# Kernel tuning notes

Measured on AMD Instinct MI355X. Metric: run time of the kernel, lower is better.

The kernel has to match this reference:

```python
import jax, jax.numpy as jnp
import numpy as np

B, S, D, H, DK, NQ, DFF = 4, 2048, 512, 8, 64, 4, 2048
EPS = 1e-5  # torch LayerNorm default


def setup_inputs() -> dict:
    key = jax.random.key(0)
    ks = jax.random.split(key, 8)
    sc = 1.0 / np.sqrt(D)
    inp = {"x": jax.random.normal(ks[0], (B, S, D), jnp.float32)}
    inp["wq"] = jax.random.normal(ks[1], (D, D), jnp.float32) * sc
    inp["bq"] = jnp.zeros((D,), jnp.float32)
    inp["wk"] = jax.random.normal(ks[2], (D, D), jnp.float32) * sc
    inp["bk"] = jnp.zeros((D,), jnp.float32)
    inp["wv"] = jax.random.normal(ks[3], (D, D), jnp.float32) * sc
    inp["bv"] = jnp.zeros((D,), jnp.float32)
    inp["wo"] = jax.random.normal(ks[4], (D, D), jnp.float32) * sc
    inp["bo"] = jnp.zeros((D,), jnp.float32)
    inp["w1"] = jax.random.normal(ks[5], (D, DFF), jnp.float32) * sc
    inp["b1"] = jnp.zeros((DFF,), jnp.float32)
    inp["w2"] = jax.random.normal(ks[6], (DFF, D), jnp.float32) * (1.0 / np.sqrt(DFF))
    inp["b2"] = jnp.zeros((D,), jnp.float32)
    inp["g1"] = jnp.ones((D,), jnp.float32)
    inp["be1"] = jnp.zeros((D,), jnp.float32)
    inp["g2"] = jnp.ones((D,), jnp.float32)
    inp["be2"] = jnp.zeros((D,), jnp.float32)
    return inp


def _layernorm(x, g, b):
    m = x.mean(-1, keepdims=True)
    v = ((x - m) ** 2).mean(-1, keepdims=True)
    return (x - m) * jax.lax.rsqrt(v + EPS) * g + b


def _forward(x, wq, bq, wk, bk, wv, bv, wo, bo, w1, b1, w2, b2, g1, be1, g2, be2):
    Bx, Sx, Dx = x.shape

    def heads(w, b):  # [B,S,D] -> [B,H,S,DK]
        return (x @ w + b).reshape(Bx, Sx, H, DK).transpose(0, 2, 1, 3)

    q, k, v = heads(wq, bq), heads(wk, bk), heads(wv, bv)
    # Quantum circuit 'execute' yields a uniform distribution over 2^NQ bitstrings,
    # so score = E_s[(qn.s)(kn.s)] = 0.25*(sum(qn)*sum(kn) + qn.kn) over the first
    # NQ components of each head slice (closed form of the original Python loops).
    qn, kn = q[..., :NQ], k[..., :NQ]
    scores = 0.25 * (
        qn.sum(-1)[..., :, None] * kn.sum(-1)[..., None, :]
        + jnp.einsum('bhin,bhjn->bhij', qn, kn)
    )
    attn = jax.nn.softmax(scores, axis=-1)  # [B,H,S,S]
    o = jnp.einsum('bhij,bhjd->bhid', attn, v)
    o = o.transpose(0, 2, 1, 3).reshape(Bx, Sx, Dx) @ wo + bo
    x1 = _layernorm(x + o, g1, be1)  # dropout is identity in eval
    ff = jax.nn.relu(x1 @ w1 + b1) @ w2 + b2
    return _layernorm(x1 + ff, g2, be2)


def reference(x, wq, bq, wk, bk, wv, bv, wo, bo, w1, b1, w2, b2, g1, be1, g2, be2):
    return _forward(x, wq, bq, wk, bk, wv, bv, wo, bo, w1, b1, w2, b2, g1, be1, g2, be2)
```

## Files before the change

kernel.cpp:

```cpp
#include <hip/hip_runtime.h>
#include <cstdint>

#define B_   4
#define S_   2048
#define D_   512
#define H_   8
#define DFF_ 2048

typedef __attribute__((ext_vector_type(4))) float  f32x4;
typedef __attribute__((ext_vector_type(4))) int    i32x4;
typedef __attribute__((ext_vector_type(2))) unsigned int u32x2;
typedef __attribute__((ext_vector_type(4))) unsigned int u32x4;
typedef __attribute__((ext_vector_type(8))) unsigned short u16x8;

__device__ inline void mfma_bf16(f32x4& acc, i32x4 a, i32x4 b) {
  asm("v_mfma_f32_16x16x32_bf16 %0, %1, %2, %0" : "+v"(acc) : "v"(a), "v"(b));
}
__device__ inline unsigned cvt_pk_bf16(float lo, float hi) {
  unsigned r;
  asm("v_cvt_pk_bf16_f32 %0, %1, %2" : "=v"(r) : "v"(lo), "v"(hi));
  return r;
}
__device__ inline unsigned short f2b(float f) {
  unsigned u = __builtin_bit_cast(unsigned, f);
  u += 0x7fffu + ((u >> 16) & 1u);
  return (unsigned short)(u >> 16);
}
__device__ inline float b2f(unsigned short u) {
  return __builtin_bit_cast(float, ((unsigned)u) << 16);
}
__device__ inline void gload_lds16(const void* g, void* l) {
  __builtin_amdgcn_global_load_lds(
      (const __attribute__((address_space(1))) void*)g,
      (__attribute__((address_space(3))) void*)l, 16, 0, 0);
}

__global__ __launch_bounds__(256) void convx_kernel(const float* __restrict__ x,
                                                    unsigned short* __restrict__ xb) {
  size_t i = ((size_t)blockIdx.x * 256 + threadIdx.x) * 8;
  f32x4 a = *(const f32x4*)(x + i);
  f32x4 b = *(const f32x4*)(x + i + 4);
  u32x4 o = {cvt_pk_bf16(a[0], a[1]), cvt_pk_bf16(a[2], a[3]),
             cvt_pk_bf16(b[0], b[1]), cvt_pk_bf16(b[2], b[3])};
  *(u32x4*)(xb + i) = o;
}

__global__ __launch_bounds__(256) void tconv_kernel(const float* __restrict__ src,
                                                    unsigned short* __restrict__ dst,
                                                    int RK, int CN) {
  __shared__ float t[64][65];
  const int tr0 = blockIdx.y * 64, tc0 = blockIdx.x * 64;
  const int c4 = (threadIdx.x & 15) * 4, rr = threadIdx.x >> 4;
#pragma unroll
  for (int i = 0; i < 4; ++i) {
    int r = i * 16 + rr;
    f32x4 v = *(const f32x4*)(src + (size_t)(tr0 + r) * CN + tc0 + c4);
    t[r][c4] = v[0]; t[r][c4 + 1] = v[1]; t[r][c4 + 2] = v[2]; t[r][c4 + 3] = v[3];
  }
  __syncthreads();
#pragma unroll
  for (int i = 0; i < 4; ++i) {
    int oc = i * 16 + rr;
    unsigned lo = cvt_pk_bf16(t[c4][oc], t[c4 + 1][oc]);
    unsigned hi = cvt_pk_bf16(t[c4 + 2][oc], t[c4 + 3][oc]);
    u32x2 pk = {lo, hi};
    *(u32x2*)(dst + (size_t)(tc0 + oc) * RK + tr0 + c4) = pk;
  }
}

__global__ __launch_bounds__(256) void wqk_kernel(const float* __restrict__ wq,
                                                  const float* __restrict__ bq,
                                                  const float* __restrict__ wk,
                                                  const float* __restrict__ bk,
                                                  unsigned short* __restrict__ wqkb,
                                                  float* __restrict__ biasqk) {
  int c = blockIdx.x;
  const float* w; const float* bb; int scol;
  if (c < 32) { w = wq; bb = bq; scol = (c >> 2) * 64 + (c & 3); }
  else { int c2 = c - 32; w = wk; bb = bk; scol = (c2 >> 2) * 64 + (c2 & 3); }
  for (int k = threadIdx.x; k < 512; k += 256)
    wqkb[c * 512 + k] = f2b(w[(size_t)k * 512 + scol]);
  if (threadIdx.x == 0) biasqk[c] = bb[scol];
}

template<int WM, int WN, int FM, int FN, int EPI>
__global__ __launch_bounds__(256) void gemm_kernel(
    const unsigned short* __restrict__ A, const unsigned short* __restrict__ Bt,
    const float* __restrict__ bias, void* __restrict__ Cout,
    int M, int N, int K) {
  constexpr int BM = WM * FM * 16, BN = WN * FN * 16;
  constexpr int ACH = BM * 4, TCH = (BM + BN) * 4;
  constexpr int BUFSZ = (BM + BN) * 64;
  __shared__ alignas(16) char lds[2][BUFSZ];
  const int tid = threadIdx.x, lane = tid & 63;
  const int wv = tid >> 6, wr = wv / WN, wc = wv % WN;
  const int bm0 = blockIdx.y * BM, bn0 = blockIdx.x * BN;
  const int l16 = lane & 15, lg = lane >> 4;

  auto stage = [&](int buf, int k0) {
#pragma unroll
    for (int i = 0; i < TCH / 256; ++i) {
      int ci = i * 256 + tid;
      const unsigned short* src;
      if (ci < ACH) {
        int r = ci >> 2, gs = ci & 3, g = gs ^ ((r >> 1) & 3);
        src = A + (size_t)(bm0 + r) * K + k0 + g * 8;
      } else {
        int cj = ci - ACH;
        int r = cj >> 2, gs = cj & 3, g = gs ^ ((r >> 1) & 3);
        src = Bt + (size_t)(bn0 + r) * K + k0 + g * 8;
      }
      gload_lds16(src, &lds[buf][ci * 16]);
    }
  };

  f32x4 acc[FM][FN];
#pragma unroll
  for (int i = 0; i < FM; ++i)
#pragma unroll
    for (int j = 0; j < FN; ++j) acc[i][j] = (f32x4){0.f, 0.f, 0.f, 0.f};

  stage(0, 0);
  __syncthreads();
  int cur = 0;
  for (int k0 = 0; k0 < K; k0 += 32) {
    if (k0 + 32 < K) stage(cur ^ 1, k0 + 32);

    i32x4 af[FM], bf[FN];
#pragma unroll
    for (int fm = 0; fm < FM; ++fm) {
      int r = wr * FM * 16 + fm * 16 + l16;
      int gs = lg ^ ((r >> 1) & 3);
      af[fm] = *(const i32x4*)(&lds[cur][r * 64 + gs * 16]);
    }
#pragma unroll
    for (int fn = 0; fn < FN; ++fn) {
      int r = wc * FN * 16 + fn * 16 + l16;
      int gs = lg ^ ((r >> 1) & 3);
      bf[fn] = *(const i32x4*)(&lds[cur][BM * 64 + r * 64 + gs * 16]);
    }
    __builtin_amdgcn_s_setprio(1);
#pragma unroll
    for (int fm = 0; fm < FM; ++fm)
#pragma unroll
      for (int fn = 0; fn < FN; ++fn)
        mfma_bf16(acc[fm][fn], af[fm], bf[fn]);
    __builtin_amdgcn_s_setprio(0);
    __syncthreads();
    cur ^= 1;
  }

#pragma unroll
  for (int fm = 0; fm < FM; ++fm) {
#pragma unroll
    for (int fn = 0; fn < FN; ++fn) {
      f32x4 a = acc[fm][fn];
      int gm = bm0 + wr * FM * 16 + fm * 16 + lg * 4;
      int gn = bn0 + wc * FN * 16 + fn * 16 + l16;
      float bz = bias[gn];
      if constexpr (EPI == 0) {
        float* C = (float*)Cout;
#pragma unroll
        for (int r = 0; r < 4; ++r) C[(size_t)(gm + r) * N + gn] = a[r] + bz;
      } else if constexpr (EPI == 1 || EPI == 2) {
        unsigned short* C = (unsigned short*)Cout;
#pragma unroll
        for (int r = 0; r < 4; ++r) {
          float v = a[r] + bz;
          if constexpr (EPI == 2) v = fmaxf(v, 0.f);
          C[(size_t)(gm + r) * N + gn] = f2b(v);
        }
      } else {
        unsigned short* C = (unsigned short*)Cout;
        int b = gm >> 11, s = gm & 2047;
        int h = gn >> 6, d = gn & 63;
        u32x2 pk = {cvt_pk_bf16(a[0] + bz, a[1] + bz),
                    cvt_pk_bf16(a[2] + bz, a[3] + bz)};
        *(u32x2*)(C + (((size_t)(b * 8 + h)) * 64 + d) * 2048 + s) = pk;
      }
    }
  }
}

__global__ __launch_bounds__(256) void qkfin_kernel(const float* __restrict__ qk,
                                                    float* __restrict__ qt,
                                                    float* __restrict__ kh) {
  int row = blockIdx.x * 4 + (threadIdx.x >> 6);
  int lane = threadIdx.x & 63;
  float v = qk[(size_t)row * 64 + lane];
  float s4 = v + __shfl_xor(v, 1);
  s4 += __shfl_xor(s4, 2);
  int b = row >> 11, s = row & 2047;
  if (lane < 32) {
    int h = lane >> 2, n = lane & 3;
    qt[(((size_t)(b * 8 + h)) * 2048 + s) * 4 + n] = 0.25f * v;
  } else {
    int c = lane - 32, h = c >> 2, n = c & 3;
    kh[(((size_t)(b * 8 + h)) * 2048 + s) * 4 + n] = v + s4;
  }
}

__global__ __launch_bounds__(256) void attn_kernel(
    const float* __restrict__ qt, const float* __restrict__ kh,
    const unsigned short* __restrict__ vt, unsigned short* __restrict__ O) {
  __shared__ alignas(16) char vlds[2][8192];
  const int tid = threadIdx.x, lane = tid & 63, wv = tid >> 6;
  const int L = blockIdx.x;
  const int x8 = L & 7, r8 = L >> 3;
  const int bh = x8 + 8 * (r8 & 3), qblk = r8 >> 2;
  const int b = bh >> 3, h = bh & 7;
  const int i0 = qblk * 64;
  const int l16 = lane & 15, g = lane >> 4;
  const int qrow = i0 + wv * 16 + l16;
  const float4 q = *(const float4*)(qt + ((size_t)bh * 2048 + qrow) * 4);
  const float* khb = kh + (size_t)bh * 2048 * 4;
  const unsigned short* vtb = vt + (size_t)bh * 64 * 2048;

  auto stage = [&](int buf, int j0) {
#pragma unroll
    for (int i = 0; i < 2; ++i) {
      int ci = i * 256 + tid;
      int d = ci >> 3, gs = ci & 7, gg = gs ^ (d & 7);
      gload_lds16(vtb + (size_t)d * 2048 + j0 + gg * 8, &vlds[buf][ci * 16]);
    }
  };

  f32x4 acc[4];
#pragma unroll
  for (int i = 0; i < 4; ++i) acc[i] = (f32x4){0.f, 0.f, 0.f, 0.f};
  float lsum = 0.f;

  stage(0, 0);
  __syncthreads();
  int cur = 0;
  for (int j0 = 0; j0 < S_; j0 += 64) {
    if (j0 + 64 < S_) stage(cur ^ 1, j0 + 64);

#pragma unroll
    for (int ks = 0; ks < 2; ++ks) {
      const int kbase = j0 + ks * 32 + g * 8;
      float p[8];
#pragma unroll
      for (int jj = 0; jj < 8; ++jj) {
        float4 kv = *(const float4*)(khb + (size_t)(kbase + jj) * 4);
        float s = q.x * kv.x + q.y * kv.y + q.z * kv.z + q.w * kv.w;
        p[jj] = __expf(s);
        lsum += p[jj];
      }
      i32x4 pb = {(int)cvt_pk_bf16(p[0], p[1]), (int)cvt_pk_bf16(p[2], p[3]),
                  (int)cvt_pk_bf16(p[4], p[5]), (int)cvt_pk_bf16(p[6], p[7])};
      __builtin_amdgcn_s_setprio(1);
#pragma unroll
      for (int dt = 0; dt < 4; ++dt) {
        int d = dt * 16 + l16;
        int gg = (ks * 4 + g) ^ (d & 7);
        i32x4 av = *(const i32x4*)(&vlds[cur][d * 128 + gg * 16]);
        mfma_bf16(acc[dt], av, pb);
      }
      __builtin_amdgcn_s_setprio(0);
    }
    __syncthreads();
    cur ^= 1;
  }

  lsum += __shfl_xor(lsum, 16);
  lsum += __shfl_xor(lsum, 32);
  const float rin = __fdividef(1.f, lsum);
  unsigned short* ob = O + ((size_t)(b * 2048 + qrow)) * 512 + h * 64;
#pragma unroll
  for (int dt = 0; dt < 4; ++dt) {
    f32x4 o = acc[dt] * rin;
    u32x2 pk = {cvt_pk_bf16(o[0], o[1]), cvt_pk_bf16(o[2], o[3])};
    *(u32x2*)(ob + dt * 16 + g * 4) = pk;
  }
}

__global__ __launch_bounds__(256) void ln1_kernel(const float* __restrict__ x,
                                                  const unsigned short* __restrict__ ob,
                                                  const float* __restrict__ g,
                                                  const float* __restrict__ be,
                                                  unsigned short* __restrict__ x1b) {
  const int row = blockIdx.x * 4 + (threadIdx.x >> 6), lane = threadIdx.x & 63;
  const float* xr = x + (size_t)row * 512 + lane * 8;
  f32x4 a0 = *(const f32x4*)xr, a1 = *(const f32x4*)(xr + 4);
  u16x8 rb = *(const u16x8*)(ob + (size_t)row * 512 + lane * 8);
  float v[8];
#pragma unroll
  for (int i = 0; i < 4; ++i) v[i] = a0[i] + b2f(rb[i]);
#pragma unroll
  for (int i = 0; i < 4; ++i) v[4 + i] = a1[i] + b2f(rb[4 + i]);
  float sum = 0.f;
#pragma unroll
  for (int i = 0; i < 8; ++i) sum += v[i];
#pragma unroll
  for (int m = 1; m < 64; m <<= 1) sum += __shfl_xor(sum, m);
  const float mean = sum * (1.f / 512.f);
  float vs = 0.f;
#pragma unroll
  for (int i = 0; i < 8; ++i) { v[i] -= mean; vs += v[i] * v[i]; }
#pragma unroll
  for (int m = 1; m < 64; m <<= 1) vs += __shfl_xor(vs, m);
  const float rs = rsqrtf(vs * (1.f / 512.f) + 1e-5f);
  const f32x4 g0 = *(const f32x4*)(g + lane * 8), g1 = *(const f32x4*)(g + lane * 8 + 4);
  const f32x4 b0 = *(const f32x4*)(be + lane * 8), b1 = *(const f32x4*)(be + lane * 8 + 4);
  float o[8];
#pragma unroll
  for (int i = 0; i < 4; ++i) o[i] = v[i] * rs * g0[i] + b0[i];
#pragma unroll
  for (int i = 0; i < 4; ++i) o[4 + i] = v[4 + i] * rs * g1[i] + b1[i];
  u32x4 pk = {cvt_pk_bf16(o[0], o[1]), cvt_pk_bf16(o[2], o[3]),
              cvt_pk_bf16(o[4], o[5]), cvt_pk_bf16(o[6], o[7])};
  *(u32x4*)(x1b + (size_t)row * 512 + lane * 8) = pk;
}

__global__ __launch_bounds__(256) void ln2_kernel(const unsigned short* __restrict__ x1b,
                                                  float* __restrict__ io,
                                                  const float* __restrict__ g,
                                                  const float* __restrict__ be) {
  const int row = blockIdx.x * 4 + (threadIdx.x >> 6), lane = threadIdx.x & 63;
  float* r = io + (size_t)row * 512 + lane * 8;
  f32x4 a0 = *(const f32x4*)r, a1 = *(const f32x4*)(r + 4);
  u16x8 rb = *(const u16x8*)(x1b + (size_t)row * 512 + lane * 8);
  float v[8];
#pragma unroll
  for (int i = 0; i < 4; ++i) v[i] = a0[i] + b2f(rb[i]);
#pragma unroll
  for (int i = 0; i < 4; ++i) v[4 + i] = a1[i] + b2f(rb[4 + i]);
  float sum = 0.f;
#pragma unroll
  for (int i = 0; i < 8; ++i) sum += v[i];
#pragma unroll
  for (int m = 1; m < 64; m <<= 1) sum += __shfl_xor(sum, m);
  const float mean = sum * (1.f / 512.f);
  float vs = 0.f;
#pragma unroll
  for (int i = 0; i < 8; ++i) { v[i] -= mean; vs += v[i] * v[i]; }
#pragma unroll
  for (int m = 1; m < 64; m <<= 1) vs += __shfl_xor(vs, m);
  const float rs = rsqrtf(vs * (1.f / 512.f) + 1e-5f);
  const f32x4 g0 = *(const f32x4*)(g + lane * 8), g1 = *(const f32x4*)(g + lane * 8 + 4);
  const f32x4 b0 = *(const f32x4*)(be + lane * 8), b1 = *(const f32x4*)(be + lane * 8 + 4);
  f32x4 o0, o1;
#pragma unroll
  for (int i = 0; i < 4; ++i) o0[i] = v[i] * rs * g0[i] + b0[i];
#pragma unroll
  for (int i = 0; i < 4; ++i) o1[i] = v[4 + i] * rs * g1[i] + b1[i];
  *(f32x4*)r = o0;
  *(f32x4*)(r + 4) = o1;
}

extern "C" void kernel_launch(void* const* d_in, const int* in_sizes, int n_in,
                              void* d_out, int out_size, void* d_ws, size_t ws_size,
                              hipStream_t stream) {
  const float* x   = (const float*)d_in[0];
  const float* wq  = (const float*)d_in[1];
  const float* bq  = (const float*)d_in[2];
  const float* wk  = (const float*)d_in[3];
  const float* bk  = (const float*)d_in[4];
  const float* wv  = (const float*)d_in[5];
  const float* bv  = (const float*)d_in[6];
  const float* wo  = (const float*)d_in[7];
  const float* bo  = (const float*)d_in[8];
  const float* w1  = (const float*)d_in[9];
  const float* b1  = (const float*)d_in[10];
  const float* w2  = (const float*)d_in[11];
  const float* b2  = (const float*)d_in[12];
  const float* g1  = (const float*)d_in[13];
  const float* be1 = (const float*)d_in[14];
  const float* g2  = (const float*)d_in[15];
  const float* be2 = (const float*)d_in[16];
  float* out = (float*)d_out;
  char* ws = (char*)d_ws;

  unsigned short* wvb  = (unsigned short*)(ws + 0x000000);
  unsigned short* wob  = (unsigned short*)(ws + 0x080000);
  unsigned short* w1b  = (unsigned short*)(ws + 0x100000);
  unsigned short* w2b  = (unsigned short*)(ws + 0x300000);
  unsigned short* wqkb = (unsigned short*)(ws + 0x500000);
  float*          bqk  = (float*)         (ws + 0x520000);
  float*          qt   = (float*)         (ws + 0x540000);
  float*          kh   = (float*)         (ws + 0x640000);
  unsigned short* x1b  = (unsigned short*)(ws + 0x740000);
  unsigned short* xb     = (unsigned short*)(ws + 0xF40000);
  unsigned short* Ob     = (unsigned short*)(ws + 0xF40000);
  unsigned short* hidden = (unsigned short*)(ws + 0xF40000);
  float*          qkout  = (float*)         (ws + 0x1740000);
  unsigned short* vtb    = (unsigned short*)(ws + 0x1740000);
  unsigned short* oprojb = (unsigned short*)(ws + 0x1740000);

  convx_kernel<<<2048, 256, 0, stream>>>(x, xb);
  tconv_kernel<<<dim3(8, 8),  256, 0, stream>>>(wv, wvb, 512, 512);
  tconv_kernel<<<dim3(8, 8),  256, 0, stream>>>(wo, wob, 512, 512);
  tconv_kernel<<<dim3(32, 8), 256, 0, stream>>>(w1, w1b, 512, 2048);
  tconv_kernel<<<dim3(8, 32), 256, 0, stream>>>(w2, w2b, 2048, 512);
  wqk_kernel<<<64, 256, 0, stream>>>(wq, bq, wk, bk, wqkb, bqk);

  gemm_kernel<2, 2, 2, 2, 0><<<dim3(1, 128), 256, 0, stream>>>(xb, wqkb, bqk, qkout, 8192, 64, 512);
  qkfin_kernel<<<2048, 256, 0, stream>>>(qkout, qt, kh);

  gemm_kernel<2, 2, 4, 2, 3><<<dim3(8, 64), 256, 0, stream>>>(xb, wvb, bv, vtb, 8192, 512, 512);

  attn_kernel<<<1024, 256, 0, stream>>>(qt, kh, vtb, Ob);

  gemm_kernel<2, 2, 4, 2, 1><<<dim3(8, 64), 256, 0, stream>>>(Ob, wob, bo, oprojb, 8192, 512, 512);

  ln1_kernel<<<2048, 256, 0, stream>>>(x, oprojb, g1, be1, x1b);

  for (int c = 0; c < 2; ++c) {
    const unsigned short* x1c = x1b + (size_t)c * 4096 * 512;
    float* outc = out + (size_t)c * 4096 * 512;
    gemm_kernel<2, 2, 4, 4, 2><<<dim3(16, 32), 256, 0, stream>>>(x1c, w1b, b1, hidden, 4096, 2048, 512);
    gemm_kernel<2, 2, 2, 2, 0><<<dim3(8, 64), 256, 0, stream>>>(hidden, w2b, b2, outc, 4096, 512, 2048);
  }

  ln2_kernel<<<2048, 256, 0, stream>>>(x1b, out, g2, be2);
}
```

Baseline: 232.9 us.

## Triple-buffer GEMM and attention loads, fuse prep kernels and QK finalize epilogue

The six weight/input conversion kernels are merged into one prep_kernel launch, and the qkfin pass is folded into a new GEMM epilogue that writes qt/kh directly. The GEMM and attention main loops move from double to triple buffering with explicit vmcnt waits and raw barriers, so loads run two tiles ahead. Attention also stages the kh tiles into LDS via global_load_lds instead of reading them from global memory in the inner loop. The cost is more LDS per block, which may lower occupancy, and the hand-written waitcnt counts must match the number of issued loads exactly.

```diff
diff --git a/kernel.cpp b/kernel.cpp
--- a/kernel.cpp
+++ b/kernel.cpp
@@ -13,6 +13,9 @@
 typedef __attribute__((ext_vector_type(4))) unsigned int u32x4;
 typedef __attribute__((ext_vector_type(8))) unsigned short u16x8;
 
+#define VMCNT(n)    asm volatile("s_waitcnt vmcnt(" #n ")" ::: "memory")
+#define BARRIER_RAW asm volatile("s_barrier" ::: "memory")
+
 __device__ inline void mfma_bf16(f32x4& acc, i32x4 a, i32x4 b) {
   asm("v_mfma_f32_16x16x32_bf16 %0, %1, %2, %0" : "+v"(acc) : "v"(a), "v"(b));
 }
@@ -34,23 +37,18 @@
       (const __attribute__((address_space(1))) void*)g,
       (__attribute__((address_space(3))) void*)l, 16, 0, 0);
 }
-
-__global__ __launch_bounds__(256) void convx_kernel(const float* __restrict__ x,
-                                                    unsigned short* __restrict__ xb) {
-  size_t i = ((size_t)blockIdx.x * 256 + threadIdx.x) * 8;
-  f32x4 a = *(const f32x4*)(x + i);
-  f32x4 b = *(const f32x4*)(x + i + 4);
-  u32x4 o = {cvt_pk_bf16(a[0], a[1]), cvt_pk_bf16(a[2], a[3]),
-             cvt_pk_bf16(b[0], b[1]), cvt_pk_bf16(b[2], b[3])};
-  *(u32x4*)(xb + i) = o;
-}
-
-__global__ __launch_bounds__(256) void tconv_kernel(const float* __restrict__ src,
-                                                    unsigned short* __restrict__ dst,
-                                                    int RK, int CN) {
-  __shared__ float t[64][65];
-  const int tr0 = blockIdx.y * 64, tc0 = blockIdx.x * 64;
-  const int c4 = (threadIdx.x & 15) * 4, rr = threadIdx.x >> 4;
+__device__ inline void gload_lds4(const void* g, void* l) {
+  __builtin_amdgcn_global_load_lds(
+      (const __attribute__((address_space(1))) void*)g,
+      (__attribute__((address_space(3))) void*)l, 4, 0, 0);
+}
+
+__device__ inline void tconv_body(const float* __restrict__ src,
+                                  unsigned short* __restrict__ dst,
+                                  int RK, int CN, int bx, int by, int tid,
+                                  float (*t)[65]) {
+  const int tr0 = by * 64, tc0 = bx * 64;
+  const int c4 = (tid & 15) * 4, rr = tid >> 4;
 #pragma unroll
   for (int i = 0; i < 4; ++i) {
     int r = i * 16 + rr;
@@ -68,19 +66,46 @@
   }
 }
 
-__global__ __launch_bounds__(256) void wqk_kernel(const float* __restrict__ wq,
-                                                  const float* __restrict__ bq,
-                                                  const float* __restrict__ wk,
-                                                  const float* __restrict__ bk,
-                                                  unsigned short* __restrict__ wqkb,
-                                                  float* __restrict__ biasqk) {
-  int c = blockIdx.x;
-  const float* w; const float* bb; int scol;
-  if (c < 32) { w = wq; bb = bq; scol = (c >> 2) * 64 + (c & 3); }
-  else { int c2 = c - 32; w = wk; bb = bk; scol = (c2 >> 2) * 64 + (c2 & 3); }
-  for (int k = threadIdx.x; k < 512; k += 256)
-    wqkb[c * 512 + k] = f2b(w[(size_t)k * 512 + scol]);
-  if (threadIdx.x == 0) biasqk[c] = bb[scol];
+__global__ __launch_bounds__(256) void prep_kernel(
+    const float* __restrict__ x,
+    const float* __restrict__ wq, const float* __restrict__ bq,
+    const float* __restrict__ wk, const float* __restrict__ bk,
+    const float* __restrict__ wv, const float* __restrict__ wo,
+    const float* __restrict__ w1, const float* __restrict__ w2,
+    unsigned short* __restrict__ xb, unsigned short* __restrict__ wvb,
+    unsigned short* __restrict__ wob, unsigned short* __restrict__ w1b,
+    unsigned short* __restrict__ w2b, unsigned short* __restrict__ wqkb,
+    float* __restrict__ bqk) {
+  __shared__ float tsh[64][65];
+  const int blk = blockIdx.x, tid = threadIdx.x;
+  if (blk < 2048) {
+    size_t i = ((size_t)blk * 256 + tid) * 8;
+    f32x4 a = *(const f32x4*)(x + i);
+    f32x4 b = *(const f32x4*)(x + i + 4);
+    u32x4 o = {cvt_pk_bf16(a[0], a[1]), cvt_pk_bf16(a[2], a[3]),
+               cvt_pk_bf16(b[0], b[1]), cvt_pk_bf16(b[2], b[3])};
+    *(u32x4*)(xb + i) = o;
+  } else if (blk < 2112) {
+    int c = blk - 2048;
+    const float* w; const float* bb; int scol;
+    if (c < 32) { w = wq; bb = bq; scol = (c >> 2) * 64 + (c & 3); }
+    else { int c2 = c - 32; w = wk; bb = bk; scol = (c2 >> 2) * 64 + (c2 & 3); }
+    for (int k = tid; k < 512; k += 256)
+      wqkb[c * 512 + k] = f2b(w[(size_t)k * 512 + scol]);
+    if (tid == 0) bqk[c] = bb[scol];
+  } else if (blk < 2176) {
+    int lb = blk - 2112;
+    tconv_body(wv, wvb, 512, 512, lb & 7, lb >> 3, tid, tsh);
+  } else if (blk < 2240) {
+    int lb = blk - 2176;
+    tconv_body(wo, wob, 512, 512, lb & 7, lb >> 3, tid, tsh);
+  } else if (blk < 2496) {
+    int lb = blk - 2240;
+    tconv_body(w1, w1b, 512, 2048, lb & 31, lb >> 5, tid, tsh);
+  } else {
+    int lb = blk - 2496;
+    tconv_body(w2, w2b, 2048, 512, lb & 7, lb >> 3, tid, tsh);
+  }
 }
 
 template<int WM, int WN, int FM, int FN, int EPI>
@@ -90,8 +115,9 @@
     int M, int N, int K) {
   constexpr int BM = WM * FM * 16, BN = WN * FN * 16;
   constexpr int ACH = BM * 4, TCH = (BM + BN) * 4;
+  constexpr int NS = TCH / 256;
   constexpr int BUFSZ = (BM + BN) * 64;
-  __shared__ alignas(16) char lds[2][BUFSZ];
+  __shared__ alignas(16) char lds[3][BUFSZ];
   const int tid = threadIdx.x, lane = tid & 63;
   const int wv = tid >> 6, wr = wv / WN, wc = wv % WN;
   const int bm0 = blockIdx.y * BM, bn0 = blockIdx.x * BN;
@@ -99,7 +125,7 @@
 
   auto stage = [&](int buf, int k0) {
 #pragma unroll
-    for (int i = 0; i < TCH / 256; ++i) {
+    for (int i = 0; i < NS; ++i) {
       int ci = i * 256 + tid;
       const unsigned short* src;
       if (ci < ACH) {
@@ -120,11 +146,16 @@
 #pragma unroll
     for (int j = 0; j < FN; ++j) acc[i][j] = (f32x4){0.f, 0.f, 0.f, 0.f};
 
+  const int T = K >> 5;
   stage(0, 0);
-  __syncthreads();
-  int cur = 0;
-  for (int k0 = 0; k0 < K; k0 += 32) {
-    if (k0 + 32 < K) stage(cur ^ 1, k0 + 32);
+  if (T > 1) stage(1, 32);
+  if constexpr (NS == 2) VMCNT(2); else if constexpr (NS == 3) VMCNT(3); else VMCNT(4);
+  BARRIER_RAW;
+
+  for (int t = 0; t < T; ++t) {
+    const int cur = t % 3;
+    const bool more = (t + 2 < T);
+    if (more) stage((t + 2) % 3, (t + 2) << 5);
 
     i32x4 af[FM], bf[FN];
 #pragma unroll
@@ -146,8 +177,13 @@
       for (int fn = 0; fn < FN; ++fn)
         mfma_bf16(acc[fm][fn], af[fm], bf[fn]);
     __builtin_amdgcn_s_setprio(0);
-    __syncthreads();
-    cur ^= 1;
+
+    if (more) {
+      if constexpr (NS == 2) VMCNT(2); else if constexpr (NS == 3) VMCNT(3); else VMCNT(4);
+    } else {
+      VMCNT(0);
+    }
+    BARRIER_RAW;
   }
 
 #pragma unroll
@@ -170,40 +206,36 @@
           if constexpr (EPI == 2) v = fmaxf(v, 0.f);
           C[(size_t)(gm + r) * N + gn] = f2b(v);
         }
-      } else {
+      } else if constexpr (EPI == 3) {
         unsigned short* C = (unsigned short*)Cout;
         int b = gm >> 11, s = gm & 2047;
         int h = gn >> 6, d = gn & 63;
         u32x2 pk = {cvt_pk_bf16(a[0] + bz, a[1] + bz),
                     cvt_pk_bf16(a[2] + bz, a[3] + bz)};
         *(u32x2*)(C + (((size_t)(b * 8 + h)) * 64 + d) * 2048 + s) = pk;
+      } else {
+        float* qtp = (float*)Cout;
+        int c = gn & 31, hh = c >> 2, nn = c & 3;
+#pragma unroll
+        for (int r = 0; r < 4; ++r) {
+          float v = a[r] + bz;
+          float s4 = v + __shfl_xor(v, 1);
+          s4 += __shfl_xor(s4, 2);
+          int gmr = gm + r, bb = gmr >> 11, ss = gmr & 2047;
+          size_t oi = (((size_t)(bb * 8 + hh)) * 2048 + ss) * 4 + nn;
+          if (gn < 32) qtp[oi] = 0.25f * v;
+          else         qtp[262144 + oi] = v + s4;
+        }
       }
     }
-  }
-}
-
-__global__ __launch_bounds__(256) void qkfin_kernel(const float* __restrict__ qk,
-                                                    float* __restrict__ qt,
-                                                    float* __restrict__ kh) {
-  int row = blockIdx.x * 4 + (threadIdx.x >> 6);
-  int lane = threadIdx.x & 63;
-  float v = qk[(size_t)row * 64 + lane];
-  float s4 = v + __shfl_xor(v, 1);
-  s4 += __shfl_xor(s4, 2);
-  int b = row >> 11, s = row & 2047;
-  if (lane < 32) {
-    int h = lane >> 2, n = lane & 3;
-    qt[(((size_t)(b * 8 + h)) * 2048 + s) * 4 + n] = 0.25f * v;
-  } else {
-    int c = lane - 32, h = c >> 2, n = c & 3;
-    kh[(((size_t)(b * 8 + h)) * 2048 + s) * 4 + n] = v + s4;
   }
 }
 
 __global__ __launch_bounds__(256) void attn_kernel(
     const float* __restrict__ qt, const float* __restrict__ kh,
     const unsigned short* __restrict__ vt, unsigned short* __restrict__ O) {
-  __shared__ alignas(16) char vlds[2][8192];
+  __shared__ alignas(16) char vlds[3][8192];
+  __shared__ alignas(16) float khlds[3][256];
   const int tid = threadIdx.x, lane = tid & 63, wv = tid >> 6;
   const int L = blockIdx.x;
   const int x8 = L & 7, r8 = L >> 3;
@@ -223,6 +255,7 @@
       int d = ci >> 3, gs = ci & 7, gg = gs ^ (d & 7);
       gload_lds16(vtb + (size_t)d * 2048 + j0 + gg * 8, &vlds[buf][ci * 16]);
     }
+    gload_lds4(khb + (size_t)j0 * 4 + tid, &khlds[buf][tid]);
   };
 
   f32x4 acc[4];
@@ -231,19 +264,22 @@
   float lsum = 0.f;
 
   stage(0, 0);
-  __syncthreads();
-  int cur = 0;
-  for (int j0 = 0; j0 < S_; j0 += 64) {
-    if (j0 + 64 < S_) stage(cur ^ 1, j0 + 64);
+  stage(1, 64);
+  VMCNT(3);
+  BARRIER_RAW;
+
+  for (int t = 0; t < 32; ++t) {
+    const int cur = t % 3;
+    const bool more = (t + 2 < 32);
+    if (more) stage((t + 2) % 3, (t + 2) * 64);
 
 #pragma unroll
     for (int ks = 0; ks < 2; ++ks) {
-      const int kbase = j0 + ks * 32 + g * 8;
       float p[8];
 #pragma unroll
       for (int jj = 0; jj < 8; ++jj) {
-        float4 kv = *(const float4*)(khb + (size_t)(kbase + jj) * 4);
-        float s = q.x * kv.x + q.y * kv.y + q.z * kv.z + q.w * kv.w;
+        f32x4 kv = *(const f32x4*)&khlds[cur][(ks * 32 + g * 8 + jj) * 4];
+        float s = q.x * kv[0] + q.y * kv[1] + q.z * kv[2] + q.w * kv[3];
         p[jj] = __expf(s);
         lsum += p[jj];
       }
@@ -259,8 +295,9 @@
       }
       __builtin_amdgcn_s_setprio(0);
     }
-    __syncthreads();
-    cur ^= 1;
+
+    if (more) VMCNT(3); else VMCNT(0);
+    BARRIER_RAW;
   }
 
   lsum += __shfl_xor(lsum, 16);
@@ -384,19 +421,13 @@
   unsigned short* xb     = (unsigned short*)(ws + 0xF40000);
   unsigned short* Ob     = (unsigned short*)(ws + 0xF40000);
   unsigned short* hidden = (unsigned short*)(ws + 0xF40000);
-  float*          qkout  = (float*)         (ws + 0x1740000);
   unsigned short* vtb    = (unsigned short*)(ws + 0x1740000);
   unsigned short* oprojb = (unsigned short*)(ws + 0x1740000);
 
-  convx_kernel<<<2048, 256, 0, stream>>>(x, xb);
-  tconv_kernel<<<dim3(8, 8),  256, 0, stream>>>(wv, wvb, 512, 512);
-  tconv_kernel<<<dim3(8, 8),  256, 0, stream>>>(wo, wob, 512, 512);
-  tconv_kernel<<<dim3(32, 8), 256, 0, stream>>>(w1, w1b, 512, 2048);
-  tconv_kernel<<<dim3(8, 32), 256, 0, stream>>>(w2, w2b, 2048, 512);
-  wqk_kernel<<<64, 256, 0, stream>>>(wq, bq, wk, bk, wqkb, bqk);
-
-  gemm_kernel<2, 2, 2, 2, 0><<<dim3(1, 128), 256, 0, stream>>>(xb, wqkb, bqk, qkout, 8192, 64, 512);
-  qkfin_kernel<<<2048, 256, 0, stream>>>(qkout, qt, kh);
+  prep_kernel<<<2752, 256, 0, stream>>>(x, wq, bq, wk, bk, wv, wo, w1, w2,
+                                        xb, wvb, wob, w1b, w2b, wqkb, bqk);
+
+  gemm_kernel<2, 2, 2, 2, 4><<<dim3(1, 128), 256, 0, stream>>>(xb, wqkb, bqk, qt, 8192, 64, 512);
 
   gemm_kernel<2, 2, 4, 2, 3><<<dim3(8, 64), 256, 0, stream>>>(xb, wvb, bv, vtb, 8192, 512, 512);
 
```

Result: faster. 191.8 us (-17.6%).
